# Performance work log

Measured on AMD Instinct MI355X. Metric: run time of the kernel, lower is better.

Reference implementation:

```python
import jax, jax.numpy as jnp
import numpy as np

NUM_NODES = 50000
NUM_EDGES = 800000
NUM_FEATURES = 128
HIDDEN = 128
NUM_GRAPHS = 256


def gcn_conv(x, W, b, src, dst, num_nodes):
    """PyG GCNConv: add self-loops, symmetric deg normalization, scatter-add, bias."""
    h = x @ W  # [N, H]
    # add self-loops
    loop = jnp.arange(num_nodes, dtype=src.dtype)
    src_f = jnp.concatenate([src, loop])
    dst_f = jnp.concatenate([dst, loop])
    # degree of destination nodes (includes self-loops)
    deg = jax.ops.segment_sum(jnp.ones_like(dst_f, dtype=h.dtype), dst_f,
                              num_segments=num_nodes)
    dinv = jnp.where(deg > 0, jax.lax.rsqrt(deg), 0.0)
    norm = dinv[src_f] * dinv[dst_f]  # [E+N]
    msg = h[src_f] * norm[:, None]    # gather + scale
    out = jax.ops.segment_sum(msg, dst_f, num_segments=num_nodes)
    return out + b


def global_mean_pool(x, batch, num_graphs):
    s = jax.ops.segment_sum(x, batch, num_segments=num_graphs)
    cnt = jax.ops.segment_sum(jnp.ones((x.shape[0],), dtype=x.dtype), batch,
                              num_segments=num_graphs)
    return s / jnp.maximum(cnt, 1.0)[:, None]


def setup_inputs() -> dict:
    key = jax.random.key(0)
    ks = jax.random.split(key, 8)
    x = jax.random.normal(ks[0], (NUM_NODES, NUM_FEATURES), dtype=jnp.float32)
    edge_index = jax.random.randint(ks[1], (2, NUM_EDGES), 0, NUM_NODES, dtype=jnp.int64)
    batch = jax.random.randint(ks[2], (NUM_NODES,), 0, NUM_GRAPHS, dtype=jnp.int64)
    # glorot-ish init for weights
    s1 = 1.0 / np.sqrt(NUM_FEATURES)
    s2 = 1.0 / np.sqrt(HIDDEN)
    W1 = jax.random.normal(ks[3], (NUM_FEATURES, HIDDEN), dtype=jnp.float32) * s1
    b1 = jnp.zeros((HIDDEN,), dtype=jnp.float32)
    W2 = jax.random.normal(ks[4], (HIDDEN, HIDDEN), dtype=jnp.float32) * s2
    b2 = jnp.zeros((HIDDEN,), dtype=jnp.float32)
    lin_W = jax.random.normal(ks[5], (HIDDEN, 1), dtype=jnp.float32) * s2
    lin_b = jnp.zeros((1,), dtype=jnp.float32)
    return {"x": x, "edge_index": edge_index, "batch": batch,
            "W1": W1, "b1": b1, "W2": W2, "b2": b2,
            "lin_W": lin_W, "lin_b": lin_b}


def reference(x, edge_index, batch, W1, b1, W2, b2, lin_W, lin_b):
    src, dst = edge_index[0], edge_index[1]
    n = x.shape[0]
    h = jax.nn.relu(gcn_conv(x, W1, b1, src, dst, n))
    h = jax.nn.relu(gcn_conv(h, W2, b2, src, dst, n))
    g = global_mean_pool(h, batch, NUM_GRAPHS)  # [G, H]
    return g @ lin_W + lin_b                    # [G, 1]
```

## Files before the change

kernel.cpp:

```cpp
#include <hip/hip_runtime.h>

#define NFEAT 128
#define NPART 64
#define NAUX  128
#define CAP   64

typedef unsigned int uint;
typedef __attribute__((ext_vector_type(8))) short short8v;
typedef __attribute__((ext_vector_type(8))) unsigned short ushort8v;
typedef __attribute__((ext_vector_type(4))) float floatx4;

__device__ inline float bf2f(unsigned short u) {
    return __uint_as_float(((uint)u) << 16);
}
__device__ inline unsigned short f2bf(float f) {
    uint u = __float_as_uint(f);
    return (unsigned short)((u + 0x7fffu + ((u >> 16) & 1u)) >> 16);
}

__global__ __launch_bounds__(256) void zero_kernel(int4* __restrict__ p, int n4) {
    int i = blockIdx.x * 256 + threadIdx.x;
    int stride = gridDim.x * 256;
    int4 z = make_int4(0, 0, 0, 0);
    for (; i < n4; i += stride) p[i] = z;
}

__global__ void prep_kernel(const int* __restrict__ src, const int* __restrict__ dst,
                            const int* __restrict__ batch,
                            const float* __restrict__ W1, const float* __restrict__ W2,
                            int* __restrict__ cnt, unsigned short* __restrict__ csr,
                            unsigned short* __restrict__ wt, float* __restrict__ gcntp,
                            int E, int N) {
    if (blockIdx.x < 4096) {
        const int shard = blockIdx.x & 7;
        const int blk = blockIdx.x >> 3;
        const int span = (N + 7) >> 3;
        const int lo = shard * span;
        const int hi = min(N, lo + span);
        const int stride = 512 * 256;
        for (int e = blk * 256 + (int)threadIdx.x; e < E; e += stride) {
            int d = __builtin_nontemporal_load(dst + e);
            if (d >= lo && d < hi) {
                int pos = atomicAdd(&cnt[d], 1);
                if (pos < CAP)
                    csr[d * CAP + pos] = (unsigned short)__builtin_nontemporal_load(src + e);
            }
        }
    } else {
        const int ab = blockIdx.x - 4096;
        const int tid = threadIdx.x;
        const int idx = ab * 256 + tid;
        {
            const float* W = (idx < 16384) ? W1 : W2;
            int i = idx & 16383;
            int k = i >> 7, n = i & 127;
            float v = W[k * 128 + n];
            unsigned short h = f2bf(v);
            unsigned short l = f2bf(v - bf2f(h));
            unsigned short* base = wt + (idx < 16384 ? 0 : 2) * 16384;
            base[n * 128 + k] = h;
            base[16384 + n * 128 + k] = l;
        }
        __shared__ int hist[256];
        hist[tid] = 0;
        __syncthreads();
        const int per = (N + NAUX - 1) / NAUX;
        const int lo2 = ab * per;
        const int hi2 = min(N, lo2 + per);
        for (int v = lo2 + tid; v < hi2; v += 256) atomicAdd(&hist[batch[v]], 1);
        __syncthreads();
        gcntp[ab * 256 + tid] = (float)hist[tid];
    }
}

__global__ __launch_bounds__(256) void gemm1_mfma_kernel(const float* __restrict__ X,
                                                         const unsigned short* __restrict__ wt,
                                                         const int* __restrict__ cnt,
                                                         unsigned short* __restrict__ out,
                                                         int nrows) {
    __shared__ unsigned short xs_hi[64][72], xs_lo[64][72];
    const int tid = threadIdx.x;
    const int w = tid >> 6, lane = tid & 63;
    const int nl = lane & 15, kg = lane >> 4;
    const int row0 = blockIdx.x * 64;

    floatx4 acc[8];
#pragma unroll
    for (int nt = 0; nt < 8; ++nt) acc[nt] = (floatx4){0.f, 0.f, 0.f, 0.f};

    for (int p = 0; p < 2; ++p) {
        __syncthreads();
        for (int idx = tid; idx < 64 * 16; idx += 256) {
            int r = idx >> 4, q = idx & 15;
            float4 v = make_float4(0.f, 0.f, 0.f, 0.f);
            if (row0 + r < nrows)
                v = ((const float4*)(X + (size_t)(row0 + r) * NFEAT + p * 64))[q];
            ushort4 h, l;
            h.x = f2bf(v.x); l.x = f2bf(v.x - bf2f(h.x));
            h.y = f2bf(v.y); l.y = f2bf(v.y - bf2f(h.y));
            h.z = f2bf(v.z); l.z = f2bf(v.z - bf2f(h.z));
            h.w = f2bf(v.w); l.w = f2bf(v.w - bf2f(h.w));
            *(ushort4*)&xs_hi[r][q * 4] = h;
            *(ushort4*)&xs_lo[r][q * 4] = l;
        }
        __syncthreads();
#pragma unroll
        for (int kc = 0; kc < 2; ++kc) {
            const int k8 = kc * 32 + kg * 8;
            const int kgl = p * 64 + k8;
            short8v ah = *(const short8v*)&xs_hi[w * 16 + nl][k8];
            short8v al = *(const short8v*)&xs_lo[w * 16 + nl][k8];
#pragma unroll
            for (int nt = 0; nt < 8; ++nt) {
                short8v bh = *(const short8v*)(wt + (size_t)(nt * 16 + nl) * 128 + kgl);
                short8v bl = *(const short8v*)(wt + 16384 + (size_t)(nt * 16 + nl) * 128 + kgl);
                acc[nt] = __builtin_amdgcn_mfma_f32_16x16x32_bf16(ah, bh, acc[nt], 0, 0, 0);
                acc[nt] = __builtin_amdgcn_mfma_f32_16x16x32_bf16(al, bh, acc[nt], 0, 0, 0);
                acc[nt] = __builtin_amdgcn_mfma_f32_16x16x32_bf16(ah, bl, acc[nt], 0, 0, 0);
            }
        }
    }
    const int rbase = row0 + w * 16 + kg * 4;
#pragma unroll
    for (int reg = 0; reg < 4; ++reg) {
        int grow = rbase + reg;
        if (grow < nrows) {
            float dv = rsqrtf((float)(cnt[grow] + 1));
#pragma unroll
            for (int nt = 0; nt < 8; ++nt)
                out[(size_t)grow * NFEAT + nt * 16 + nl] = f2bf(acc[nt][reg] * dv);
        }
    }
}

__global__ __launch_bounds__(256) void gemm2_mfma_kernel(const unsigned short* __restrict__ X,
                                                         const unsigned short* __restrict__ wt,
                                                         const int* __restrict__ cnt,
                                                         unsigned short* __restrict__ out,
                                                         int nrows) {
    __shared__ unsigned short xs[64][72];
    const int tid = threadIdx.x;
    const int w = tid >> 6, lane = tid & 63;
    const int nl = lane & 15, kg = lane >> 4;
    const int row0 = blockIdx.x * 64;

    floatx4 acc[8];
#pragma unroll
    for (int nt = 0; nt < 8; ++nt) acc[nt] = (floatx4){0.f, 0.f, 0.f, 0.f};

    for (int p = 0; p < 2; ++p) {
        __syncthreads();
        for (int idx = tid; idx < 64 * 8; idx += 256) {
            int r = idx >> 3, q = idx & 7;
            short8v v = {0, 0, 0, 0, 0, 0, 0, 0};
            if (row0 + r < nrows)
                v = *(const short8v*)(X + (size_t)(row0 + r) * NFEAT + p * 64 + q * 8);
            *(short8v*)&xs[r][q * 8] = v;
        }
        __syncthreads();
#pragma unroll
        for (int kc = 0; kc < 2; ++kc) {
            const int k8 = kc * 32 + kg * 8;
            const int kgl = p * 64 + k8;
            short8v a = *(const short8v*)&xs[w * 16 + nl][k8];
#pragma unroll
            for (int nt = 0; nt < 8; ++nt) {
                short8v bh = *(const short8v*)(wt + (size_t)(nt * 16 + nl) * 128 + kgl);
                short8v bl = *(const short8v*)(wt + 16384 + (size_t)(nt * 16 + nl) * 128 + kgl);
                acc[nt] = __builtin_amdgcn_mfma_f32_16x16x32_bf16(a, bh, acc[nt], 0, 0, 0);
                acc[nt] = __builtin_amdgcn_mfma_f32_16x16x32_bf16(a, bl, acc[nt], 0, 0, 0);
            }
        }
    }
    const int rbase = row0 + w * 16 + kg * 4;
#pragma unroll
    for (int reg = 0; reg < 4; ++reg) {
        int grow = rbase + reg;
        if (grow < nrows) {
            float dv = rsqrtf((float)(cnt[grow] + 1));
#pragma unroll
            for (int nt = 0; nt < 8; ++nt)
                out[(size_t)grow * NFEAT + nt * 16 + nl] = f2bf(acc[nt][reg] * dv);
        }
    }
}

__device__ inline void agg_gather8(const ushort8v* __restrict__ hp8,
                                   const unsigned short* __restrict__ csr,
                                   int v, int d, int ep, int q, float acc[8]) {
    const int s = v * CAP;
    if (ep == 0) {
        ushort8v r = hp8[(size_t)v * 16 + q];
#pragma unroll
        for (int k = 0; k < 8; ++k) acc[k] += bf2f(r[k]);
    }
    int i = 0;
    for (; i + 16 <= d; i += 16) {
        int u[4];
#pragma unroll
        for (int j = 0; j < 4; ++j) u[j] = csr[s + i + 4 * j + ep];
        ushort8v a[4];
#pragma unroll
        for (int j = 0; j < 4; ++j) a[j] = hp8[(size_t)u[j] * 16 + q];
#pragma unroll
        for (int j = 0; j < 4; ++j)
#pragma unroll
            for (int k = 0; k < 8; ++k) acc[k] += bf2f(a[j][k]);
    }
    if (i < d) {
        int u[4];
#pragma unroll
        for (int j = 0; j < 4; ++j) {
            int e = i + 4 * j + ep;
            u[j] = csr[s + (e < d ? e : d - 1)];
        }
        ushort8v a[4];
#pragma unroll
        for (int j = 0; j < 4; ++j) a[j] = hp8[(size_t)u[j] * 16 + q];
#pragma unroll
        for (int j = 0; j < 4; ++j) {
            if (i + 4 * j + ep < d) {
#pragma unroll
                for (int k = 0; k < 8; ++k) acc[k] += bf2f(a[j][k]);
            }
        }
    }
#pragma unroll
    for (int k = 0; k < 8; ++k) {
        acc[k] += __shfl_xor(acc[k], 16);
        acc[k] += __shfl_xor(acc[k], 32);
    }
}

__global__ __launch_bounds__(256) void agg_relu_kernel(const ushort8v* __restrict__ hp8,
                                                       const int* __restrict__ cnt,
                                                       const unsigned short* __restrict__ csr,
                                                       const float* __restrict__ bias,
                                                       unsigned short* __restrict__ out,
                                                       int N, int npw) {
    const int wgl = (blockIdx.x * 256 + threadIdx.x) >> 6;
    const int lane = threadIdx.x & 63;
    const int ep = lane >> 4;
    const int q = lane & 15;
    float4 bb0 = *(const float4*)(bias + q * 8);
    float4 bb1 = *(const float4*)(bias + q * 8 + 4);
    const int v0 = wgl * npw;
    const int v1 = min(N, v0 + npw);
    for (int v = v0; v < v1; ++v) {
        int d = cnt[v];
        float acc[8] = {0, 0, 0, 0, 0, 0, 0, 0};
        agg_gather8(hp8, csr, v, d, ep, q, acc);
        if (ep == 0) {
            const float dv = rsqrtf((float)(d + 1));
            ushort8v o;
            o[0] = f2bf(fmaxf(fmaf(acc[0], dv, bb0.x), 0.f));
            o[1] = f2bf(fmaxf(fmaf(acc[1], dv, bb0.y), 0.f));
            o[2] = f2bf(fmaxf(fmaf(acc[2], dv, bb0.z), 0.f));
            o[3] = f2bf(fmaxf(fmaf(acc[3], dv, bb0.w), 0.f));
            o[4] = f2bf(fmaxf(fmaf(acc[4], dv, bb1.x), 0.f));
            o[5] = f2bf(fmaxf(fmaf(acc[5], dv, bb1.y), 0.f));
            o[6] = f2bf(fmaxf(fmaf(acc[6], dv, bb1.z), 0.f));
            o[7] = f2bf(fmaxf(fmaf(acc[7], dv, bb1.w), 0.f));
            *(ushort8v*)(out + (size_t)v * NFEAT + q * 8) = o;
        }
    }
}

__global__ __launch_bounds__(256) void agg_pool_kernel(const ushort8v* __restrict__ hp8,
                                                       const int* __restrict__ cnt,
                                                       const unsigned short* __restrict__ csr,
                                                       const float* __restrict__ bias,
                                                       const float* __restrict__ linW,
                                                       const int* __restrict__ batch,
                                                       float* __restrict__ gpart,
                                                       int N, int npw) {
    const int wgl = (blockIdx.x * 256 + threadIdx.x) >> 6;
    const int lane = threadIdx.x & 63;
    const int ep = lane >> 4;
    const int q = lane & 15;
    float4 bb0 = *(const float4*)(bias + q * 8);
    float4 bb1 = *(const float4*)(bias + q * 8 + 4);
    float4 lw0 = *(const float4*)(linW + q * 8);
    float4 lw1 = *(const float4*)(linW + q * 8 + 4);
    const int v0 = wgl * npw;
    const int v1 = min(N, v0 + npw);
    for (int v = v0; v < v1; ++v) {
        int d = cnt[v];
        float acc[8] = {0, 0, 0, 0, 0, 0, 0, 0};
        agg_gather8(hp8, csr, v, d, ep, q, acc);
        const float dv = rsqrtf((float)(d + 1));
        float sc = fmaxf(fmaf(acc[0], dv, bb0.x), 0.f) * lw0.x
                 + fmaxf(fmaf(acc[1], dv, bb0.y), 0.f) * lw0.y
                 + fmaxf(fmaf(acc[2], dv, bb0.z), 0.f) * lw0.z
                 + fmaxf(fmaf(acc[3], dv, bb0.w), 0.f) * lw0.w
                 + fmaxf(fmaf(acc[4], dv, bb1.x), 0.f) * lw1.x
                 + fmaxf(fmaf(acc[5], dv, bb1.y), 0.f) * lw1.y
                 + fmaxf(fmaf(acc[6], dv, bb1.z), 0.f) * lw1.z
                 + fmaxf(fmaf(acc[7], dv, bb1.w), 0.f) * lw1.w;
        sc += __shfl_xor(sc, 1);
        sc += __shfl_xor(sc, 2);
        sc += __shfl_xor(sc, 4);
        sc += __shfl_xor(sc, 8);
        if (lane == 0) atomicAdd(&gpart[(v & (NPART - 1)) * 256 + batch[v]], sc);
    }
}

__global__ void finalize_kernel(const float* __restrict__ gpart, const float* __restrict__ gcntp,
                                const float* __restrict__ linb, float* __restrict__ out, int G) {
    int g = threadIdx.x;
    if (g < G) {
        float s = 0.f;
        for (int p = 0; p < NPART; ++p) s += gpart[p * 256 + g];
        float c = 0.f;
        for (int b = 0; b < NAUX; ++b) c += gcntp[b * 256 + g];
        out[g] = s / fmaxf(c, 1.0f) + linb[0];
    }
}

extern "C" void kernel_launch(void* const* d_in, const int* in_sizes, int n_in,
                              void* d_out, int out_size, void* d_ws, size_t ws_size,
                              hipStream_t stream) {
    const float* x    = (const float*)d_in[0];
    const int*   eidx = (const int*)d_in[1];
    const int*   batch= (const int*)d_in[2];
    const float* W1   = (const float*)d_in[3];
    const float* b1   = (const float*)d_in[4];
    const float* W2   = (const float*)d_in[5];
    const float* b2   = (const float*)d_in[6];
    const float* linW = (const float*)d_in[7];
    const float* linb = (const float*)d_in[8];
    float* out = (float*)d_out;

    const int N = in_sizes[0] / NFEAT;
    const int E = in_sizes[1] / 2;
    const int G = out_size;
    const int* src = eidx;
    const int* dst = eidx + E;

    char* p = (char*)d_ws;
    unsigned short* hpBf  = (unsigned short*)p; p += (size_t)N * NFEAT * sizeof(unsigned short);
    unsigned short* h1Bf  = (unsigned short*)p; p += (size_t)N * NFEAT * sizeof(unsigned short);
    unsigned short* hp2Bf = (unsigned short*)p; p += (size_t)N * NFEAT * sizeof(unsigned short);
    unsigned short* csr   = (unsigned short*)p; p += (size_t)N * CAP * sizeof(unsigned short);
    unsigned short* wt    = (unsigned short*)p; p += (size_t)4 * 16384 * sizeof(unsigned short);
    int*   cnt   = (int*)p;   p += (size_t)N * sizeof(int);
    float* gpart = (float*)p; p += (size_t)NPART * 256 * sizeof(float);
    float* gcntp = (float*)p; p += (size_t)NAUX * 256 * sizeof(float);
    (void)ws_size; (void)n_in;

    const int nz4 = (int)(((size_t)(N + NPART * 256) * 4 + 15) / 16);
    zero_kernel<<<256, 256, 0, stream>>>((int4*)cnt, nz4);

    prep_kernel<<<4096 + NAUX, 256, 0, stream>>>(src, dst, batch, W1, W2, cnt, csr, wt,
                                                 gcntp, E, N);

    const int NWAVE = 2048 * 4;
    const int npw = (N + NWAVE - 1) / NWAVE;

    gemm1_mfma_kernel<<<(N + 63) / 64, 256, 0, stream>>>(x, wt, cnt, hpBf, N);
    agg_relu_kernel<<<2048, 256, 0, stream>>>((const ushort8v*)hpBf, cnt, csr,
                                              b1, h1Bf, N, npw);
    gemm2_mfma_kernel<<<(N + 63) / 64, 256, 0, stream>>>(h1Bf, wt + 2 * 16384, cnt, hp2Bf, N);
    agg_pool_kernel<<<2048, 256, 0, stream>>>((const ushort8v*)hp2Bf, cnt, csr,
                                              b2, linW, batch, gpart, N, npw);
    finalize_kernel<<<1, 256, 0, stream>>>(gpart, gcntp, linb, out, G);
}
```

Before: 186.1 us.

## Replace 8-pass sharded CSR build with two-phase bucket binning

The old prep kernel read the full dst array eight times, once per destination shard, and filtered edges to localise atomics. The new scheme bins edges once into eight packed per-shard buckets (local offset and source in one word) using block-local staging and one global atomic per bucket per tile. A second kernel then scatters each bucket into the CSR with per-node atomics. It also reuses the hpBf buffer for the second GEMM output. It adds a kernel launch and a bucket buffer with a fixed capacity, which could overflow if a shard receives more than 131072 edges.

```diff
diff --git a/kernel.cpp b/kernel.cpp
--- a/kernel.cpp
+++ b/kernel.cpp
@@ -4,6 +4,8 @@
 #define NPART 64
 #define NAUX  128
 #define CAP   64
+#define NBINBLK 1563
+#define BCAP  131072
 
 typedef unsigned int uint;
 typedef __attribute__((ext_vector_type(8))) short short8v;
@@ -25,29 +27,66 @@
     for (; i < n4; i += stride) p[i] = z;
 }
 
-__global__ void prep_kernel(const int* __restrict__ src, const int* __restrict__ dst,
-                            const int* __restrict__ batch,
-                            const float* __restrict__ W1, const float* __restrict__ W2,
-                            int* __restrict__ cnt, unsigned short* __restrict__ csr,
-                            unsigned short* __restrict__ wt, float* __restrict__ gcntp,
-                            int E, int N) {
-    if (blockIdx.x < 4096) {
-        const int shard = blockIdx.x & 7;
-        const int blk = blockIdx.x >> 3;
+__global__ __launch_bounds__(256) void binA_kernel(const int* __restrict__ src,
+                                                   const int* __restrict__ dst,
+                                                   const int* __restrict__ batch,
+                                                   const float* __restrict__ W1,
+                                                   const float* __restrict__ W2,
+                                                   uint* __restrict__ bucket,
+                                                   int* __restrict__ gcur,
+                                                   unsigned short* __restrict__ wt,
+                                                   float* __restrict__ gcntp,
+                                                   int E, int N) {
+    if (blockIdx.x < NBINBLK) {
+        __shared__ int lcnt[8], lbase[8], gbase[8], lofs[8];
+        __shared__ uint stage[512];
         const int span = (N + 7) >> 3;
-        const int lo = shard * span;
-        const int hi = min(N, lo + span);
-        const int stride = 512 * 256;
-        for (int e = blk * 256 + (int)threadIdx.x; e < E; e += stride) {
-            int d = __builtin_nontemporal_load(dst + e);
-            if (d >= lo && d < hi) {
-                int pos = atomicAdd(&cnt[d], 1);
-                if (pos < CAP)
-                    csr[d * CAP + pos] = (unsigned short)__builtin_nontemporal_load(src + e);
-            }
+        const int tid = threadIdx.x;
+        for (int t = blockIdx.x; t * 512 < E; t += NBINBLK) {
+            const int e0 = t * 512;
+            const int n = min(512, E - e0);
+            if (tid < 8) { lcnt[tid] = 0; lofs[tid] = 0; }
+            __syncthreads();
+            int myb[2]; uint myv[2];
+#pragma unroll
+            for (int j = 0; j < 2; ++j) {
+                int e = e0 + j * 256 + tid;
+                myb[j] = -1;
+                if (e < E) {
+                    int d = dst[e];
+                    int s = src[e];
+                    int b = (int)((uint)d / (uint)span);
+                    myb[j] = b;
+                    myv[j] = ((uint)(d - b * span) << 16) | (uint)s;
+                    atomicAdd(&lcnt[b], 1);
+                }
+            }
+            __syncthreads();
+            if (tid == 0) {
+                int r = 0;
+                for (int b = 0; b < 8; ++b) { lbase[b] = r; r += lcnt[b]; }
+            }
+            __syncthreads();
+            if (tid < 8 && lcnt[tid] > 0) gbase[tid] = atomicAdd(&gcur[tid], lcnt[tid]);
+            __syncthreads();
+#pragma unroll
+            for (int j = 0; j < 2; ++j) {
+                if (myb[j] >= 0) {
+                    int p = lbase[myb[j]] + atomicAdd(&lofs[myb[j]], 1);
+                    stage[p] = myv[j];
+                }
+            }
+            __syncthreads();
+            for (int i = tid; i < n; i += 256) {
+                int b = 0;
+                while (b < 7 && i >= lbase[b + 1]) ++b;
+                int gp = gbase[b] + (i - lbase[b]);
+                if (gp < BCAP) bucket[(size_t)b * BCAP + gp] = stage[i];
+            }
+            __syncthreads();
         }
     } else {
-        const int ab = blockIdx.x - 4096;
+        const int ab = blockIdx.x - NBINBLK;
         const int tid = threadIdx.x;
         const int idx = ab * 256 + tid;
         {
@@ -70,6 +109,24 @@
         for (int v = lo2 + tid; v < hi2; v += 256) atomicAdd(&hist[batch[v]], 1);
         __syncthreads();
         gcntp[ab * 256 + tid] = (float)hist[tid];
+    }
+}
+
+__global__ __launch_bounds__(256) void binB_kernel(const uint* __restrict__ bucket,
+                                                   const int* __restrict__ gcur,
+                                                   int* __restrict__ cnt,
+                                                   unsigned short* __restrict__ csr, int N) {
+    const int s = blockIdx.x & 7;
+    const int blk = blockIdx.x >> 3;
+    const int span = (N + 7) >> 3;
+    const int lo = s * span;
+    const int len = min(gcur[s], BCAP);
+    const uint* bsrc = bucket + (size_t)s * BCAP;
+    for (int i = blk * 256 + (int)threadIdx.x; i < len; i += 512 * 256) {
+        uint v = bsrc[i];
+        int d = lo + (int)(v >> 16);
+        int pos = atomicAdd(&cnt[d], 1);
+        if (pos < CAP) csr[d * CAP + pos] = (unsigned short)(v & 0xFFFFu);
     }
 }
 
@@ -340,19 +397,21 @@
     char* p = (char*)d_ws;
     unsigned short* hpBf  = (unsigned short*)p; p += (size_t)N * NFEAT * sizeof(unsigned short);
     unsigned short* h1Bf  = (unsigned short*)p; p += (size_t)N * NFEAT * sizeof(unsigned short);
-    unsigned short* hp2Bf = (unsigned short*)p; p += (size_t)N * NFEAT * sizeof(unsigned short);
     unsigned short* csr   = (unsigned short*)p; p += (size_t)N * CAP * sizeof(unsigned short);
     unsigned short* wt    = (unsigned short*)p; p += (size_t)4 * 16384 * sizeof(unsigned short);
-    int*   cnt   = (int*)p;   p += (size_t)N * sizeof(int);
-    float* gpart = (float*)p; p += (size_t)NPART * 256 * sizeof(float);
-    float* gcntp = (float*)p; p += (size_t)NAUX * 256 * sizeof(float);
+    int*   cnt    = (int*)p;   p += (size_t)N * sizeof(int);
+    float* gpart  = (float*)p; p += (size_t)NPART * 256 * sizeof(float);
+    int*   gcur   = (int*)p;   p += 16 * sizeof(int);
+    float* gcntp  = (float*)p; p += (size_t)NAUX * 256 * sizeof(float);
+    uint*  bucket = (uint*)p;  p += (size_t)8 * BCAP * sizeof(uint);
     (void)ws_size; (void)n_in;
 
-    const int nz4 = (int)(((size_t)(N + NPART * 256) * 4 + 15) / 16);
+    const int nz4 = (int)(((size_t)(N + NPART * 256 + 16) * 4 + 15) / 16);
     zero_kernel<<<256, 256, 0, stream>>>((int4*)cnt, nz4);
 
-    prep_kernel<<<4096 + NAUX, 256, 0, stream>>>(src, dst, batch, W1, W2, cnt, csr, wt,
-                                                 gcntp, E, N);
+    binA_kernel<<<NBINBLK + NAUX, 256, 0, stream>>>(src, dst, batch, W1, W2, bucket, gcur,
+                                                    wt, gcntp, E, N);
+    binB_kernel<<<4096, 256, 0, stream>>>(bucket, gcur, cnt, csr, N);
 
     const int NWAVE = 2048 * 4;
     const int npw = (N + NWAVE - 1) / NWAVE;
@@ -360,8 +419,8 @@
     gemm1_mfma_kernel<<<(N + 63) / 64, 256, 0, stream>>>(x, wt, cnt, hpBf, N);
     agg_relu_kernel<<<2048, 256, 0, stream>>>((const ushort8v*)hpBf, cnt, csr,
                                               b1, h1Bf, N, npw);
-    gemm2_mfma_kernel<<<(N + 63) / 64, 256, 0, stream>>>(h1Bf, wt + 2 * 16384, cnt, hp2Bf, N);
-    agg_pool_kernel<<<2048, 256, 0, stream>>>((const ushort8v*)hp2Bf, cnt, csr,
+    gemm2_mfma_kernel<<<(N + 63) / 64, 256, 0, stream>>>(h1Bf, wt + 2 * 16384, cnt, hpBf, N);
+    agg_pool_kernel<<<2048, 256, 0, stream>>>((const ushort8v*)hpBf, cnt, csr,
                                               b2, linW, batch, gpart, N, npw);
     finalize_kernel<<<1, 256, 0, stream>>>(gpart, gcntp, linb, out, G);
 }
```

Result: slower. 206.8 us (+11.1%).
